# Performance work log

Hardware: AMD Instinct MI355X
Metric: run time of the kernel (lower is better)

## Reference

```python
import jax, jax.numpy as jnp
import numpy as np

# 5x5 binomial Gaussian kernel, normalized by 256
_K = jnp.array([[1., 4., 6., 4., 1.],
                [4., 16., 24., 16., 4.],
                [6., 24., 36., 24., 6.],
                [4., 16., 24., 16., 4.],
                [1., 4., 6., 4., 1.]], dtype=jnp.float32) / 256.0


def _gauss_conv(img, kernel):
    # depthwise 5x5 conv with reflect padding 2 (same spatial size)
    C = img.shape[1]
    p = jnp.pad(img, ((0, 0), (0, 0), (2, 2), (2, 2)), mode='reflect')
    return jax.lax.conv_general_dilated(
        p, kernel, window_strides=(1, 1), padding='VALID',
        dimension_numbers=('NCHW', 'OIHW', 'NCHW'),
        feature_group_count=C)


def _lap_pyramid(img, kernel, max_levels=5):
    pyr = []
    cur = img
    for _ in range(max_levels):  # fixed small loop over pyramid levels
        H, W = cur.shape[2], cur.shape[3]
        cur = cur[:, :, :H - H % 2, :W - W % 2]  # crop to even size
        down = _gauss_conv(cur, kernel)[:, :, ::2, ::2]
        up = jnp.zeros(cur.shape, cur.dtype).at[:, :, ::2, ::2].set(down * 4.0)
        up = _gauss_conv(up, kernel)
        pyr.append(cur - up)
        cur = down
    return pyr


def setup_inputs() -> dict:
    key = jax.random.key(0)
    k1, k2 = jax.random.split(key)
    predict = jax.random.uniform(k1, (16, 3, 512, 512), dtype=jnp.float32)
    target = jax.random.uniform(k2, (16, 3, 512, 512), dtype=jnp.float32)
    return {"predict": predict, "target": target}


def reference(predict, target):
    C = predict.shape[1]
    kernel = jnp.tile(_K.astype(predict.dtype)[None, None], (C, 1, 1, 1))  # [C,1,5,5]
    pyr_p = _lap_pyramid(predict, kernel, 5)
    pyr_t = _lap_pyramid(target, kernel, 5)
    weights = (1.0, 2.0, 4.0, 8.0, 16.0)
    loss = jnp.asarray(0.0, predict.dtype)
    for w, a, b in zip(weights, pyr_p, pyr_t):
        loss = loss + w * jnp.mean(jnp.abs(a - b))  # F.l1_loss (mean reduction)
    return loss
```

## Files before the change

### kernel.cpp

```cpp
#include <hip/hip_runtime.h>


__device__ __forceinline__ int reflect_i(int m, int S) {
    if (m < 0) m = -m;
    if (m >= S) m = 2 * S - 2 - m;
    return m;
}

__device__ __forceinline__ void wg_barrier() {
    asm volatile("s_waitcnt lgkmcnt(0)" ::: "memory");
    __builtin_amdgcn_s_barrier();
}

#define LGKM0 asm volatile("s_waitcnt lgkmcnt(0)" ::: "memory")

template <int N>
__device__ __forceinline__ void wait_vm() {
    if constexpr (N == 0)      asm volatile("s_waitcnt vmcnt(0)" ::: "memory");
    else if constexpr (N == 1) asm volatile("s_waitcnt vmcnt(1)" ::: "memory");
    else if constexpr (N == 2) asm volatile("s_waitcnt vmcnt(2)" ::: "memory");
    else if constexpr (N == 4) asm volatile("s_waitcnt vmcnt(4)" ::: "memory");
    else if constexpr (N == 8) asm volatile("s_waitcnt vmcnt(8)" ::: "memory");
}

__device__ __forceinline__ void gld16(const void* g, void* l) {
    __builtin_amdgcn_global_load_lds(
        (const __attribute__((address_space(1))) void*)g,
        (__attribute__((address_space(3))) void*)l, 16, 0, 0);
}

template <int S, int ISL0, int DH>
__global__ __launch_bounds__(256, 2)
void pyr_kernel(const float* __restrict__ a, const float* __restrict__ b,
                float* __restrict__ dwn, float* __restrict__ acc, float scale) {
    constexpr int D = S / 2;
    constexpr int CPL = S / 128;
    constexpr int ROWB = (CPL == 4) ? 2048 : 1024;
    constexpr int SLOT = ROWB * (ISL0 ? 2 : 1);
    constexpr int OPS = (CPL == 4) ? (ISL0 ? 4 : 2) : 1;
    constexpr int NRS = D / DH;

    __shared__ float4 ringmem[4 * 4 * SLOT / 16];
    const int wv = threadIdx.x >> 6;
    const int lane = threadIdx.x & 63;
    char* ring = (char*)ringmem + wv * (4 * SLOT);

    const int wid = blockIdx.x * 4 + wv;
    const int rs = wid % NRS;
    const int n = wid / NRS;
    const int R0 = rs * DH;
    const size_t gbase = (size_t)n * S * S;

    auto stage_row = [&](int s) {
        int gr = reflect_i(2 * R0 - 4 + s, S);
        const char* ga = (const char*)(a + gbase + (size_t)gr * S);
        char* la = ring + (s & 3) * SLOT;
        if constexpr (CPL == 4) {
            gld16(ga + 16 * lane, la);
            gld16(ga + 16 * lane + 1024, la + 1024);
        } else if constexpr (CPL == 2) {
            gld16(ga + 16 * lane, la);
        } else {
            gld16(ga + 16 * (lane & 31), la);
        }
        if constexpr (ISL0) {
            const char* gb = (const char*)(b + gbase + (size_t)gr * S);
            gld16(gb + 16 * lane, la + ROWB);
            gld16(gb + 16 * lane + 1024, la + ROWB + 1024);
        }
    };

    auto proc_row = [&](int s, float* c, float* h) {
        const char* pa = ring + (s & 3) * SLOT;
        if constexpr (CPL == 4) {
            float4 x0 = *(const float4*)(pa + 16 * lane);
            float4 x1 = *(const float4*)(pa + 1024 + 16 * lane);
            if constexpr (ISL0) {
                const char* pb = pa + ROWB;
                float4 y0 = *(const float4*)(pb + 16 * lane);
                float4 y1 = *(const float4*)(pb + 1024 + 16 * lane);
                x0.x -= y0.x; x0.y -= y0.y; x0.z -= y0.z; x0.w -= y0.w;
                x1.x -= y1.x; x1.y -= y1.y; x1.z -= y1.z; x1.w -= y1.w;
            }
            c[0]=x0.x; c[1]=x0.y; c[2]=x0.z; c[3]=x0.w;
            c[4]=x1.x; c[5]=x1.y; c[6]=x1.z; c[7]=x1.w;
            float lu2  = __shfl_up(x0.z, 1, 64);
            float lu3  = __shfl_up(x0.w, 1, 64);
            float rd0  = __shfl_down(x0.x, 1, 64);
            float bcA  = __shfl(x1.x, 0, 64);
            float lu2b = __shfl_up(x1.z, 1, 64);
            float lu3b = __shfl_up(x1.w, 1, 64);
            float rd0b = __shfl_down(x1.x, 1, 64);
            float bcZ  = __shfl(x0.z, 63, 64);
            float bcW  = __shfl(x0.w, 63, 64);
            float w0 = (lane == 0) ? x0.z : lu2;
            float w1 = (lane == 0) ? x0.y : lu3;
            float w6 = (lane == 63) ? bcA : rd0;
            float v0 = (lane == 0) ? bcZ : lu2b;
            float v1 = (lane == 0) ? bcW : lu3b;
            float v6 = (lane == 63) ? x1.z : rd0b;
            h[0] = w0 + 4.f*w1 + 6.f*x0.x + 4.f*x0.y + x0.z;
            h[1] = x0.x + 4.f*x0.y + 6.f*x0.z + 4.f*x0.w + w6;
            h[2] = v0 + 4.f*v1 + 6.f*x1.x + 4.f*x1.y + x1.z;
            h[3] = x1.x + 4.f*x1.y + 6.f*x1.z + 4.f*x1.w + v6;
        } else if constexpr (CPL == 2) {
            float4 x0 = *(const float4*)(pa + 16 * lane);
            c[0]=x0.x; c[1]=x0.y; c[2]=x0.z; c[3]=x0.w;
            float lu2 = __shfl_up(x0.z, 1, 64);
            float lu3 = __shfl_up(x0.w, 1, 64);
            float rd0 = __shfl_down(x0.x, 1, 64);
            float w0 = (lane == 0) ? x0.z : lu2;
            float w1 = (lane == 0) ? x0.y : lu3;
            float w6 = (lane == 63) ? x0.z : rd0;
            h[0] = w0 + 4.f*w1 + 6.f*x0.x + 4.f*x0.y + x0.z;
            h[1] = x0.x + 4.f*x0.y + 6.f*x0.z + 4.f*x0.w + w6;
        } else {
            float2 x0 = *(const float2*)(pa + 8 * lane);
            c[0]=x0.x; c[1]=x0.y;
            float lu0 = __shfl_up(x0.x, 1, 64);
            float lu1 = __shfl_up(x0.y, 1, 64);
            float rd0 = __shfl_down(x0.x, 1, 64);
            float w0 = (lane == 0) ? rd0 : lu0;
            float w1 = (lane == 0) ? x0.y : lu1;
            float w4 = (lane == 63) ? x0.x : rd0;
            h[0] = w0 + 4.f*w1 + 6.f*x0.x + 4.f*x0.y + w4;
        }
    };

    float hA[CPL], hB[CPL], hC[CPL], hD[CPL], hE[CPL];
    float cEv1[2*CPL], cEv2[2*CPL], cOd1[2*CPL], dump[2*CPL];
    float ex0[CPL] = {}, ex1[CPL] = {}, ox0[CPL] = {}, ox1[CPL] = {};
    float sum = 0.f;
    float* dbase = dwn + (size_t)n * D * D;

    stage_row(0); stage_row(1); stage_row(2); stage_row(3);
    wait_vm<OPS>();
    proc_row(0, dump, hA);
    proc_row(1, dump, hB);
    proc_row(2, dump, hC);
    LGKM0;
    stage_row(4); stage_row(5); stage_row(6);

    #pragma unroll
    for (int j = 0; j <= DH + 1; ++j) {
        const int m = R0 - 1 + j;
        if (j <= DH) wait_vm<2 * OPS>(); else wait_vm<0>();

        float c3[2*CPL], c4[2*CPL];
        proc_row(2 * j + 3, c3, hD);
        proc_row(2 * j + 4, c4, hE);

        float d[CPL], dl[CPL], dr[CPL], ex2[CPL], ox2[CPL];
        #pragma unroll
        for (int q = 0; q < CPL; q++)
            d[q] = (hA[q] + 4.f*hB[q] + 6.f*hC[q] + 4.f*hD[q] + hE[q]) * (1.f / 256.f);

        if constexpr (CPL == 4) {
            float su1 = __shfl_up(d[1], 1, 64);
            float su3 = __shfl_up(d[3], 1, 64);
            float sd0 = __shfl_down(d[0], 1, 64);
            float sd2 = __shfl_down(d[2], 1, 64);
            float bc1 = __shfl(d[1], 63, 64);
            float bc2 = __shfl(d[2], 0, 64);
            dl[0] = (lane == 0) ? d[1] : su1;
            dl[1] = d[0];
            dl[2] = (lane == 0) ? bc1 : su3;
            dl[3] = d[2];
            dr[0] = d[1];
            dr[1] = (lane == 63) ? bc2 : sd0;
            dr[2] = d[3];
            dr[3] = (lane == 63) ? d[3] : sd2;
        } else if constexpr (CPL == 2) {
            float su1 = __shfl_up(d[1], 1, 64);
            float sd0 = __shfl_down(d[0], 1, 64);
            dl[0] = (lane == 0) ? d[1] : su1;
            dl[1] = d[0];
            dr[0] = d[1];
            dr[1] = (lane == 63) ? d[1] : sd0;
        } else {
            float su = __shfl_up(d[0], 1, 64);
            float sd = __shfl_down(d[0], 1, 64);
            dl[0] = (lane == 0) ? sd : su;
            dr[0] = (lane == 63) ? d[0] : sd;
        }
        #pragma unroll
        for (int q = 0; q < CPL; q++) {
            ex2[q] = 0.125f * (dl[q] + 6.f * d[q] + dr[q]);
            ox2[q] = 0.5f * (d[q] + dr[q]);
        }

        if (j >= 1 && j <= DH) {
            if constexpr (CPL == 4) {
                *(float2*)(dbase + (size_t)m * D + 2 * lane) = make_float2(d[0], d[1]);
                *(float2*)(dbase + (size_t)m * D + D / 2 + 2 * lane) = make_float2(d[2], d[3]);
            } else if constexpr (CPL == 2) {
                *(float2*)(dbase + (size_t)m * D + 2 * lane) = make_float2(d[0], d[1]);
            } else {
                dbase[(size_t)m * D + lane] = d[0];
            }
        }

        if (j >= 2) {
            const int me = m - 1;
            #pragma unroll
            for (int q = 0; q < CPL; q++) {
                float eA = (me == 0) ? ex2[q] : ex0[q];
                float oA = (me == 0) ? ox2[q] : ox0[q];
                float eC = (me == D - 1) ? ex1[q] : ex2[q];
                float oC = (me == D - 1) ? ox1[q] : ox2[q];
                float uee = 0.125f * (eA + 6.f * ex1[q] + eC);
                float ueo = 0.125f * (oA + 6.f * ox1[q] + oC);
                float uoe = 0.5f * (ex1[q] + eC);
                float uoo = 0.5f * (ox1[q] + oC);
                sum += fabsf(cEv2[2*q]   - uee) + fabsf(cEv2[2*q+1] - ueo)
                     + fabsf(cOd1[2*q]   - uoe) + fabsf(cOd1[2*q+1] - uoo);
            }
        }

        #pragma unroll
        for (int q = 0; q < CPL; q++) {
            ex0[q] = ex1[q]; ex1[q] = ex2[q];
            ox0[q] = ox1[q]; ox1[q] = ox2[q];
            hA[q] = hC[q]; hB[q] = hD[q]; hC[q] = hE[q];
        }
        #pragma unroll
        for (int q = 0; q < 2 * CPL; q++) {
            cEv2[q] = cEv1[q];
            cEv1[q] = c4[q];
            cOd1[q] = c3[q];
        }

        if (j <= DH - 1) {
            LGKM0;
            stage_row(2 * j + 7);
            stage_row(2 * j + 8);
        }
    }

    #pragma unroll
    for (int o = 32; o > 0; o >>= 1) sum += __shfl_down(sum, o, 64);
    if (lane == 0) atomicAdd(&acc[wid & 63], sum * scale);
}

__device__ float level_in_lds(const float* cur, float* h, float* dn,
                              int S, int tid, int nt) {
    const int D = S >> 1;
    for (int i = tid; i < S * D; i += nt) {
        int r = i / D, xh = i % D;
        int c0 = reflect_i(2 * xh - 2, S), c1 = reflect_i(2 * xh - 1, S);
        int c3 = 2 * xh + 1, c4 = reflect_i(2 * xh + 2, S);
        const float* row = cur + r * S;
        h[i] = row[c0] + 4.f * row[c1] + 6.f * row[2 * xh] + 4.f * row[c3] + row[c4];
    }
    wg_barrier();
    for (int i = tid; i < D * D; i += nt) {
        int yh = i / D, xh = i % D;
        int r0 = reflect_i(2 * yh - 2, S), r1 = reflect_i(2 * yh - 1, S);
        int r3 = 2 * yh + 1, r4 = reflect_i(2 * yh + 2, S);
        dn[i] = (h[r0 * D + xh] + 4.f * h[r1 * D + xh] + 6.f * h[2 * yh * D + xh]
               + 4.f * h[r3 * D + xh] + h[r4 * D + xh]) * (1.f / 256.f);
    }
    wg_barrier();
    float sum = 0.f;
    for (int i = tid; i < D * D; i += nt) {
        int yh2 = i / D, q = i % D;
        int rm = (yh2 == 0) ? 1 : yh2 - 1;
        int rp = (yh2 == D - 1) ? D - 1 : yh2 + 1;
        int cm = (q == 0) ? 1 : q - 1;
        int cp = (q == D - 1) ? D - 1 : q + 1;
        float A00 = dn[rm * D + cm], A01 = dn[rm * D + q], A02 = dn[rm * D + cp];
        float A10 = dn[yh2 * D + cm], A11 = dn[yh2 * D + q], A12 = dn[yh2 * D + cp];
        float A20 = dn[rp * D + cm], A21 = dn[rp * D + q], A22 = dn[rp * D + cp];
        float ex0 = (A00 + 6.f * A01 + A02) * 0.125f;
        float ex1 = (A10 + 6.f * A11 + A12) * 0.125f;
        float ex2 = (A20 + 6.f * A21 + A22) * 0.125f;
        float ox0 = (A01 + A02) * 0.5f;
        float ox1 = (A11 + A12) * 0.5f;
        float ox2 = (A21 + A22) * 0.5f;
        float uee = (ex0 + 6.f * ex1 + ex2) * 0.125f;
        float ueo = (ox0 + 6.f * ox1 + ox2) * 0.125f;
        float uoe = (ex1 + ex2) * 0.5f;
        float uoo = (ox1 + ox2) * 0.5f;
        const float* c0 = cur + (2 * yh2) * S + 2 * q;
        sum += fabsf(c0[0] - uee) + fabsf(c0[1] - ueo)
             + fabsf(c0[S] - uoe) + fabsf(c0[S + 1] - uoo);
    }
    wg_barrier();
    return sum;
}

__global__ __launch_bounds__(256)
void tail_kernel(const float* __restrict__ d2, float* __restrict__ acc,
                 float s3, float s4) {
    __shared__ float cur[64 * 64];
    __shared__ float hbuf[64 * 32];
    __shared__ float dn3[32 * 32];
    __shared__ float dn4[16 * 16];
    int n = blockIdx.x, tid = threadIdx.x;
    const float4* src = (const float4*)(d2 + (size_t)n * 64 * 64);
    for (int i = tid; i < 64 * 16; i += 256) ((float4*)cur)[i] = src[i];
    wg_barrier();
    float sum = level_in_lds(cur, hbuf, dn3, 64, tid, 256) * s3;
    sum += level_in_lds(dn3, hbuf, dn4, 32, tid, 256) * s4;
    #pragma unroll
    for (int o = 32; o > 0; o >>= 1) sum += __shfl_down(sum, o, 64);
    __shared__ float s[4];
    int lane = tid & 63, w = tid >> 6;
    if (lane == 0) s[w] = sum;
    wg_barrier();
    if (tid == 0) atomicAdd(&acc[n & 63], s[0] + s[1] + s[2] + s[3]);
}

__global__ void finish_kernel(const float* __restrict__ acc, float* __restrict__ out) {
    float v = acc[threadIdx.x];
    #pragma unroll
    for (int o = 32; o > 0; o >>= 1) v += __shfl_down(v, o, 64);
    if (threadIdx.x == 0) out[0] = v;
}

extern "C" void kernel_launch(void* const* d_in, const int* in_sizes, int n_in,
                              void* d_out, int out_size, void* d_ws, size_t ws_size,
                              hipStream_t stream) {
    const float* p = (const float*)d_in[0];
    const float* t = (const float*)d_in[1];
    float* out = (float*)d_out;
    float* acc = (float*)d_ws;
    float* dn0 = acc + 64;
    float* dn1 = dn0 + (size_t)48 * 256 * 256;
    float* dn2 = dn1 + (size_t)48 * 128 * 128;

    hipMemsetAsync(acc, 0, 64 * sizeof(float), stream);

    const int N = 48;

    pyr_kernel<512, 1, 8><<<384, 256, 0, stream>>>(
        p, t, dn0, acc, 1.f / (float)(N * 512 * 512));
    pyr_kernel<256, 0, 8><<<192, 256, 0, stream>>>(
        dn0, nullptr, dn1, acc, 2.f / (float)(N * 256 * 256));
    pyr_kernel<128, 0, 8><<<96, 256, 0, stream>>>(
        dn1, nullptr, dn2, acc, 4.f / (float)(N * 128 * 128));
    tail_kernel<<<N, 256, 0, stream>>>(dn2, acc,
                                       8.f / (float)(N * 64 * 64),
                                       16.f / (float)(N * 32 * 32));
    finish_kernel<<<1, 64, 0, stream>>>(acc, out);
}
```

Measured before the change: 66.26 us.

## Fold level 2 into the LDS tail kernel and retile level 0 waves

The third pyramid level (128x128) now runs inside the tail kernel: each 512-thread block loads a 128x128 image into LDS and computes levels 2, 3 and 4 there, reusing buffers. This drops one kernel launch and the global write and read of the 64x64 downsampled intermediate. The level-0 pyramid kernel is also templated on waves per block and now runs with 2 waves per block, each covering 16 rows instead of 8. The tail kernel uses about 112 KB of LDS with only 48 blocks, so it runs at low occupancy and parallelism on the 128x128 level.

```diff
diff --git a/kernel.cpp b/kernel.cpp
--- a/kernel.cpp
+++ b/kernel.cpp
@@ -29,8 +29,8 @@
         (__attribute__((address_space(3))) void*)l, 16, 0, 0);
 }
 
-template <int S, int ISL0, int DH>
-__global__ __launch_bounds__(256, 2)
+template <int S, int ISL0, int DH, int WPB>
+__global__ __launch_bounds__(WPB * 64, 2)
 void pyr_kernel(const float* __restrict__ a, const float* __restrict__ b,
                 float* __restrict__ dwn, float* __restrict__ acc, float scale) {
     constexpr int D = S / 2;
@@ -40,12 +40,12 @@
     constexpr int OPS = (CPL == 4) ? (ISL0 ? 4 : 2) : 1;
     constexpr int NRS = D / DH;
 
-    __shared__ float4 ringmem[4 * 4 * SLOT / 16];
+    __shared__ float4 ringmem[WPB * 4 * SLOT / 16];
     const int wv = threadIdx.x >> 6;
     const int lane = threadIdx.x & 63;
     char* ring = (char*)ringmem + wv * (4 * SLOT);
 
-    const int wid = blockIdx.x * 4 + wv;
+    const int wid = blockIdx.x * WPB + wv;
     const int rs = wid % NRS;
     const int n = wid / NRS;
     const int R0 = rs * DH;
@@ -289,26 +289,34 @@
     return sum;
 }
 
-__global__ __launch_bounds__(256)
-void tail_kernel(const float* __restrict__ d2, float* __restrict__ acc,
-                 float s3, float s4) {
-    __shared__ float cur[64 * 64];
-    __shared__ float hbuf[64 * 32];
-    __shared__ float dn3[32 * 32];
-    __shared__ float dn4[16 * 16];
+__global__ __launch_bounds__(512, 1)
+void tail_kernel(const float* __restrict__ d1, float* __restrict__ acc,
+                 float s2, float s3, float s4) {
+    __shared__ float cur[128 * 128];
+    __shared__ float hbuf[128 * 64];
+    __shared__ float dn2[64 * 64];
     int n = blockIdx.x, tid = threadIdx.x;
-    const float4* src = (const float4*)(d2 + (size_t)n * 64 * 64);
-    for (int i = tid; i < 64 * 16; i += 256) ((float4*)cur)[i] = src[i];
-    wg_barrier();
-    float sum = level_in_lds(cur, hbuf, dn3, 64, tid, 256) * s3;
-    sum += level_in_lds(dn3, hbuf, dn4, 32, tid, 256) * s4;
+    const int nt = 512;
+    const float4* src = (const float4*)(d1 + (size_t)n * 128 * 128);
+    for (int i = tid; i < 128 * 32; i += nt) ((float4*)cur)[i] = src[i];
+    wg_barrier();
+    float sum = level_in_lds(cur, hbuf, dn2, 128, tid, nt) * s2;
+    float* dn3 = cur;
+    sum += level_in_lds(dn2, hbuf, dn3, 64, tid, nt) * s3;
+    float* dn4 = cur + 32 * 32;
+    sum += level_in_lds(dn3, hbuf, dn4, 32, tid, nt) * s4;
     #pragma unroll
     for (int o = 32; o > 0; o >>= 1) sum += __shfl_down(sum, o, 64);
-    __shared__ float s[4];
+    __shared__ float s[8];
     int lane = tid & 63, w = tid >> 6;
     if (lane == 0) s[w] = sum;
     wg_barrier();
-    if (tid == 0) atomicAdd(&acc[n & 63], s[0] + s[1] + s[2] + s[3]);
+    if (tid == 0) {
+        float v = 0.f;
+        #pragma unroll
+        for (int i = 0; i < 8; i++) v += s[i];
+        atomicAdd(&acc[n & 63], v);
+    }
 }
 
 __global__ void finish_kernel(const float* __restrict__ acc, float* __restrict__ out) {
@@ -327,19 +335,17 @@
     float* acc = (float*)d_ws;
     float* dn0 = acc + 64;
     float* dn1 = dn0 + (size_t)48 * 256 * 256;
-    float* dn2 = dn1 + (size_t)48 * 128 * 128;
 
     hipMemsetAsync(acc, 0, 64 * sizeof(float), stream);
 
     const int N = 48;
 
-    pyr_kernel<512, 1, 8><<<384, 256, 0, stream>>>(
+    pyr_kernel<512, 1, 16, 2><<<384, 128, 0, stream>>>(
         p, t, dn0, acc, 1.f / (float)(N * 512 * 512));
-    pyr_kernel<256, 0, 8><<<192, 256, 0, stream>>>(
+    pyr_kernel<256, 0, 8, 4><<<192, 256, 0, stream>>>(
         dn0, nullptr, dn1, acc, 2.f / (float)(N * 256 * 256));
-    pyr_kernel<128, 0, 8><<<96, 256, 0, stream>>>(
-        dn1, nullptr, dn2, acc, 4.f / (float)(N * 128 * 128));
-    tail_kernel<<<N, 256, 0, stream>>>(dn2, acc,
+    tail_kernel<<<N, 512, 0, stream>>>(dn1, acc,
+                                       4.f / (float)(N * 128 * 128),
                                        8.f / (float)(N * 64 * 64),
                                        16.f / (float)(N * 32 * 32));
     finish_kernel<<<1, 64, 0, stream>>>(acc, out);
```

After: 56.83 us, median of 2. 1.17x faster.
